# Kernel optimization log

Measured on AMD Instinct MI355X. Metric: run time of the kernel, lower is better.

Reference implementation:

```python
import jax, jax.numpy as jnp
import numpy as np

N = 128       # n_channels
B = 131072    # batch
C = np.float32(np.sqrt(0.5))  # 50/50 beamsplitter amplitude (c = s = sqrt(0.5))


def setup_inputs() -> dict:
    key = jax.random.key(0)
    k1, k2, k3, k4 = jax.random.split(key, 4)
    M = N * (N - 1) // 2
    return {
        "x_real": jax.random.normal(k1, (B, N), jnp.float32),
        "x_imag": jax.random.normal(k2, (B, N), jnp.float32),
        "mzi_phases": jax.random.normal(k3, (M * 2,), jnp.float32) * 0.1,
        "output_phases": jax.random.normal(k4, (N,), jnp.float32) * 0.1,
    }


def _construct_unitary(mzi_phases, output_phases):
    n = output_phases.shape[0]
    m = n * (n - 1) // 2
    # pair ordering matches the torch double loop: i ascending, then j > i (row-major triu)
    i_np, j_np = np.triu_indices(n, 1)
    i_idx = jnp.asarray(i_np, jnp.int32)
    j_idx = jnp.asarray(j_np, jnp.int32)
    ph = mzi_phases.reshape(m, 2)
    theta, phi = ph[:, 0], ph[:, 1]

    def step(U, xs):
        th, ph_, i, j = xs
        e_phi = jax.lax.complex(jnp.cos(ph_), jnp.sin(ph_))
        e_th = jax.lax.complex(jnp.cos(th), jnp.sin(th))
        ri = U[i]
        rj = U[j]
        # T_ij @ U touches only rows i and j (O(N) Givens row update)
        new_i = C * ri + (C * e_phi) * rj
        new_j = (C * e_th) * ri - (C * e_th * e_phi) * rj
        U = U.at[i].set(new_i).at[j].set(new_j)
        return U, None

    def chunk_body(U, xs_chunk):
        U, _ = jax.lax.scan(step, U, xs_chunk)
        return U, None

    # chunk the M sequential updates: M = (n-1) * (n//2) for even n;
    # checkpointing chunks keeps reverse-mode memory O(sqrt-ish) instead of O(M * N^2)
    n_chunks = n - 1
    cs = n // 2
    xs = (theta.reshape(n_chunks, cs), phi.reshape(n_chunks, cs),
          i_idx.reshape(n_chunks, cs), j_idx.reshape(n_chunks, cs))
    U0 = jnp.eye(n, dtype=jnp.complex64)
    U, _ = jax.lax.scan(jax.checkpoint(chunk_body), U0, xs)
    # output phase screen D @ U
    d = jax.lax.complex(jnp.cos(output_phases), jnp.sin(output_phases))
    return d[:, None] * U


def reference(x_real, x_imag, mzi_phases, output_phases):
    U = _construct_unitary(mzi_phases, output_phases)           # [N, N] complex64
    x = jax.lax.complex(x_real, x_imag)                          # [B, N] complex64
    # matmul(U, x.unsqueeze(-1)).squeeze(-1) == x @ U^T
    out = jnp.einsum('nm,bm->bn', U, x)                          # [B, N] complex64
    # ComplexDropout is identity in eval mode
    return out
```

## Files before the change

### kernel.cpp

```cpp
#include <hip/hip_runtime.h>
#include <hip/hip_bf16.h>

#define NDIM 128
#define BDIM 131072
#define NMZI 8128
#define NCHUNK 8
#define CSTEP (NMZI / NCHUNK)
#define NJG 8
#define NCOL 32
#define NLOC 16
static constexpr float CC = 0.70710678118654752440f;

typedef __attribute__((ext_vector_type(8))) short bf16x8;
typedef __attribute__((ext_vector_type(4))) float f32x4;

__device__ __align__(16) float2         g_V[NCHUNK * NDIM * NDIM];
__device__ __align__(16) float2         g_W[4 * NDIM * NDIM];
__device__ __align__(16) float2         g_Y[2 * NDIM * NDIM];
__device__ __align__(16) unsigned short g_TB[32 * NDIM * 8];
__device__ __align__(16) unsigned short g_Ur[16 * NDIM * 8];
__device__ __align__(16) unsigned short g_Ui[16 * NDIM * 8];

__device__ inline unsigned short f2bf(float f) {
    union { __hip_bfloat16 h; unsigned short u; } cv;
    cv.h = __float2bfloat16(f);
    return cv.u;
}

__global__ __launch_bounds__(256) void build_scan(const float* __restrict__ mzi) {
    __shared__ float2 Usm[NDIM][NCOL];
    __shared__ float4 phs[CSTEP];
    __shared__ float4 comp[NJG][NCOL];
    const int tid   = threadIdx.x;
    const int c     = tid & 31;
    const int g     = tid >> 5;
    const int col0  = blockIdx.x * NCOL;
    const int chunk = blockIdx.y;
    const int s0 = chunk * CSTEP, s1 = s0 + CSTEP;

    for (int k = g; k < NDIM; k += NJG)
        Usm[k][c] = make_float2((k == col0 + c) ? 1.f : 0.f, 0.f);
    const float2* mzp = (const float2*)mzi;
    for (int t = tid; t < CSTEP; t += 256) {
        const float2 mz = mzp[s0 + t];
        float sp, cp, st, ct;
        sincosf(mz.y, &sp, &cp);
        sincosf(mz.x, &st, &ct);
        phs[t] = make_float4(cp, sp, CC * ct, CC * st);
    }
    __syncthreads();

    int i = 0, base = 0;
    while (base + (NDIM - 1 - i) <= s0) { base += NDIM - 1 - i; ++i; }

    int s = s0;
    while (s < s1) {
        const int cnt  = NDIM - 1 - i;
        const int jA   = i + 1 + (s - base);
        const int L    = min(s1, base + cnt) - s;
        const int nloc = (L + NJG - 1) >> 3;
        const int myBeg = g * nloc;
        const int myN   = max(0, min(nloc, L - myBeg));
        const int pbase = s - s0;

        const float2 r0 = Usm[i][c];

        float2 treg[NLOC];
        float2 qth[NLOC];
        float  A = 1.f;
        float2 Bc = make_float2(0.f, 0.f);
        #pragma unroll
        for (int kk = 0; kk < NLOC; ++kk) {
            if (kk < myN) {
                const int off = myBeg + kk;
                const float4 q  = phs[pbase + off];
                const float2 rj = Usm[jA + off][c];
                const float tr = fmaf(q.x, rj.x, -q.y * rj.y);
                const float ti = fmaf(q.x, rj.y,  q.y * rj.x);
                treg[kk] = make_float2(tr, ti);
                qth[kk]  = make_float2(q.z, q.w);
                Bc.x = CC * (Bc.x + tr);
                Bc.y = CC * (Bc.y + ti);
                A *= CC;
            }
        }
        comp[g][c] = make_float4(A, Bc.x, Bc.y, 0.f);
        __syncthreads();

        float2 r = r0;
        for (int h = 0; h < g; ++h) {
            const float4 cm = comp[h][c];
            r.x = fmaf(cm.x, r.x, cm.y);
            r.y = fmaf(cm.x, r.y, cm.z);
        }

        #pragma unroll
        for (int kk = 0; kk < NLOC; ++kk) {
            if (kk < myN) {
                const float2 t = treg[kk];
                const float2 q = qth[kk];
                const float dr = r.x - t.x, di = r.y - t.y;
                const float njx = fmaf(q.x, dr, -q.y * di);
                const float njy = fmaf(q.x, di,  q.y * dr);
                Usm[jA + myBeg + kk][c] = make_float2(njx, njy);
                r.x = CC * (r.x + t.x);
                r.y = CC * (r.y + t.y);
            }
        }
        if (myN > 0 && (myBeg + myN == L))
            Usm[i][c] = r;
        __syncthreads();

        s += L;
        if (s == base + cnt) { base += cnt; ++i; }
    }

    float2* Vp = g_V + chunk * NDIM * NDIM;
    for (int k = g; k < NDIM; k += NJG)
        Vp[k * NDIM + col0 + c] = Usm[k][c];
}

__global__ __launch_bounds__(128) void compose(int level) {
    const int p = blockIdx.y, n = blockIdx.x, m = threadIdx.x;
    const float2* A; const float2* B; float2* Cout;
    if (level == 0) {
        A = g_V + (2 * p + 1) * NDIM * NDIM;
        B = g_V + (2 * p) * NDIM * NDIM;
        Cout = g_W + p * NDIM * NDIM;
    } else {
        A = g_W + (2 * p + 1) * NDIM * NDIM;
        B = g_W + (2 * p) * NDIM * NDIM;
        Cout = g_Y + p * NDIM * NDIM;
    }
    __shared__ float2 arow[NDIM];
    arow[m] = A[n * NDIM + m];
    __syncthreads();
    float cr = 0.f, ci = 0.f;
    #pragma unroll 8
    for (int k = 0; k < NDIM; ++k) {
        const float2 b = B[k * NDIM + m];
        const float2 a = arow[k];
        cr = fmaf(a.x, b.x, fmaf(-a.y, b.y, cr));
        ci = fmaf(a.x, b.y, fmaf( a.y, b.x, ci));
    }
    Cout[n * NDIM + m] = make_float2(cr, ci);
}

__global__ __launch_bounds__(128) void compose_final(const float* __restrict__ oph) {
    const int n = blockIdx.x, m = threadIdx.x;
    const float2* A = g_Y + NDIM * NDIM;
    const float2* B = g_Y;
    __shared__ float2 arow[NDIM];
    arow[m] = A[n * NDIM + m];
    __syncthreads();
    float cr = 0.f, ci = 0.f;
    #pragma unroll 8
    for (int k = 0; k < NDIM; ++k) {
        const float2 b = B[k * NDIM + m];
        const float2 a = arow[k];
        cr = fmaf(a.x, b.x, fmaf(-a.y, b.y, cr));
        ci = fmaf(a.x, b.y, fmaf( a.y, b.x, ci));
    }
    float ds, dc;
    sincosf(oph[n], &ds, &dc);
    const float vr = fmaf(cr, dc, -ci * ds);
    const float vi = fmaf(cr, ds,  ci * dc);
    const int kg = m >> 3, e = m & 7;
    g_TB[(kg * NDIM + n) * 8 + e]        = f2bf(vr);
    g_TB[((16 + kg) * NDIM + n) * 8 + e] = f2bf(-vi);
    g_Ur[(kg * NDIM + n) * 8 + e] = f2bf(vr);
    g_Ui[(kg * NDIM + n) * 8 + e] = f2bf(vi);
}

__global__ __launch_bounds__(256) void cmatmul0(const float* __restrict__ xr,
                                                const float* __restrict__ xi,
                                                float* __restrict__ out) {
    __shared__ __align__(16) char smX[4][8192];
    const int tid  = threadIdx.x;
    const int lane = tid & 63;
    const int w    = tid >> 6;
    const int r15  = lane & 15;
    const int kg4  = lane >> 4;
    const int l31  = lane & 31;
    const int lh   = lane >> 5;
    const int R    = blockIdx.x * 64 + w * 16;

    const float4* sre = (const float4*)(xr + (size_t)R * NDIM);
    const float4* sim = (const float4*)(xi + (size_t)R * NDIM);
    float4 G[16];
    #pragma unroll
    for (int p = 0; p < 8; ++p) G[p]     = sre[p * 64 + lane];
    #pragma unroll
    for (int p = 0; p < 8; ++p) G[8 + p] = sim[p * 64 + lane];

    char* buf = &smX[w][0];
    #pragma unroll
    for (int p = 0; p < 8; ++p) {
        const int row = 2 * p + lh;
        const int swz = (row & 7) << 4;
        uint2 v;
        v.x = ((unsigned)f2bf(G[p].y) << 16) | f2bf(G[p].x);
        v.y = ((unsigned)f2bf(G[p].w) << 16) | f2bf(G[p].z);
        *(uint2*)(buf + row * 512 + ((l31 * 8) ^ swz)) = v;
        v.x = ((unsigned)f2bf(G[8 + p].y) << 16) | f2bf(G[8 + p].x);
        v.y = ((unsigned)f2bf(G[8 + p].w) << 16) | f2bf(G[8 + p].z);
        *(uint2*)(buf + row * 512 + 256 + ((l31 * 8) ^ swz)) = v;
    }

    bf16x8 fx[8];
    const int rswz = (r15 & 7) << 4;
    #pragma unroll
    for (int kc = 0; kc < 8; ++kc) {
        const int off = (((kc & 3) * 64 + kg4 * 16) ^ rswz) + ((kc >= 4) ? 256 : 0);
        fx[kc] = *(const bf16x8*)(buf + r15 * 512 + off);
    }

    const bf16x8* gT = (const bf16x8*)g_TB;
    const size_t orow = (size_t)(R + r15) * NDIM;
    #pragma unroll
    for (int nt = 0; nt < 8; ++nt) {
        f32x4 a0 = {0.f, 0.f, 0.f, 0.f};
        f32x4 a1 = {0.f, 0.f, 0.f, 0.f};
        #pragma unroll
        for (int kc = 0; kc < 4; ++kc)
            a0 = __builtin_amdgcn_mfma_f32_16x16x32_bf16(
                gT[(kc * 4 + kg4) * NDIM + nt * 16 + r15], fx[kc], a0, 0, 0, 0);
        #pragma unroll
        for (int kc = 4; kc < 8; ++kc)
            a1 = __builtin_amdgcn_mfma_f32_16x16x32_bf16(
                gT[(kc * 4 + kg4) * NDIM + nt * 16 + r15], fx[kc], a1, 0, 0, 0);
        const f32x4 s = a0 + a1;
        *(float4*)(out + orow + nt * 16 + kg4 * 4) =
            make_float4(s[0], s[1], s[2], s[3]);
    }
}

__global__ __launch_bounds__(256) void cmatmul1(const float* __restrict__ xr,
                                                const float* __restrict__ xi,
                                                ushort2* __restrict__ outp) {
    const int lane  = threadIdx.x & 63;
    const int w     = threadIdx.x >> 6;
    const int btile = blockIdx.x * 64 + w * 16;
    const int r15   = lane & 15;
    const int kg4   = lane >> 4;
    const int bload = btile + r15;

    const bf16x8* Ur = (const bf16x8*)g_Ur;
    const bf16x8* Ui = (const bf16x8*)g_Ui;
    const float* xrp = xr + (size_t)bload * NDIM;
    const float* xip = xi + (size_t)bload * NDIM;

    bf16x8 ar[4], ai[4], ain[4];
    #pragma unroll
    for (int kc = 0; kc < 4; ++kc) {
        const int k0 = kc * 32 + kg4 * 8;
        float4 rlo = *(const float4*)(xrp + k0);
        float4 rhi = *(const float4*)(xrp + k0 + 4);
        float4 ilo = *(const float4*)(xip + k0);
        float4 ihi = *(const float4*)(xip + k0 + 4);
        bf16x8 vr, vi, vn;
        vr[0] = (short)f2bf(rlo.x); vr[1] = (short)f2bf(rlo.y);
        vr[2] = (short)f2bf(rlo.z); vr[3] = (short)f2bf(rlo.w);
        vr[4] = (short)f2bf(rhi.x); vr[5] = (short)f2bf(rhi.y);
        vr[6] = (short)f2bf(rhi.z); vr[7] = (short)f2bf(rhi.w);
        vi[0] = (short)f2bf(ilo.x); vi[1] = (short)f2bf(ilo.y);
        vi[2] = (short)f2bf(ilo.z); vi[3] = (short)f2bf(ilo.w);
        vi[4] = (short)f2bf(ihi.x); vi[5] = (short)f2bf(ihi.y);
        vi[6] = (short)f2bf(ihi.z); vi[7] = (short)f2bf(ihi.w);
        #pragma unroll
        for (int e = 0; e < 8; ++e) vn[e] = (short)(vi[e] ^ 0x8000);
        ar[kc] = vr; ai[kc] = vi; ain[kc] = vn;
    }

    #pragma unroll
    for (int nt = 0; nt < 8; ++nt) {
        f32x4 accR = {0.f, 0.f, 0.f, 0.f};
        f32x4 accI = {0.f, 0.f, 0.f, 0.f};
        #pragma unroll
        for (int kc = 0; kc < 4; ++kc) {
            const int kg = kc * 4 + kg4;
            bf16x8 br = Ur[kg * NDIM + nt * 16 + r15];
            bf16x8 bi = Ui[kg * NDIM + nt * 16 + r15];
            accR = __builtin_amdgcn_mfma_f32_16x16x32_bf16(ar[kc],  br, accR, 0, 0, 0);
            accR = __builtin_amdgcn_mfma_f32_16x16x32_bf16(ain[kc], bi, accR, 0, 0, 0);
            accI = __builtin_amdgcn_mfma_f32_16x16x32_bf16(ar[kc],  bi, accI, 0, 0, 0);
            accI = __builtin_amdgcn_mfma_f32_16x16x32_bf16(ai[kc],  br, accI, 0, 0, 0);
        }
        const int n    = nt * 16 + r15;
        const int brow = btile + kg4 * 4;
        #pragma unroll
        for (int r = 0; r < 4; ++r)
            outp[(size_t)(brow + r) * NDIM + n] = make_ushort2(f2bf(accR[r]), f2bf(accI[r]));
    }
}

extern "C" void kernel_launch(void* const* d_in, const int* in_sizes, int n_in,
                              void* d_out, int out_size, void* d_ws, size_t ws_size,
                              hipStream_t stream) {
    const float* xr  = (const float*)d_in[0];
    const float* xi  = (const float*)d_in[1];
    const float* mzi = (const float*)d_in[2];
    const float* oph = (const float*)d_in[3];

    build_scan<<<dim3(4, NCHUNK), dim3(256), 0, stream>>>(mzi);
    compose<<<dim3(NDIM, 4), dim3(128), 0, stream>>>(0);
    compose<<<dim3(NDIM, 2), dim3(128), 0, stream>>>(1);
    compose_final<<<dim3(NDIM), dim3(128), 0, stream>>>(oph);
    if (out_size == BDIM * NDIM) {
        cmatmul0<<<dim3(BDIM / 64), dim3(256), 0, stream>>>(xr, xi, (float*)d_out);
    } else {
        cmatmul1<<<dim3(BDIM / 64), dim3(256), 0, stream>>>(xr, xi, (ushort2*)d_out);
    }
}
```

Baseline: 122.7 us.

## Split MZI scan into more chunks and use nontemporal loads/stores in matmul

Doubles the number of parallel scan chunks in the unitary build from 8 to 16, adding one more level to the pairwise compose tree, so the serial Givens-rotation chain per block is half as long. The complex matmul kernel also switches its input loads and output stores to nontemporal builtins to reduce cache pollution on the streamed data. The cost is an extra compose launch and a larger intermediate buffer.

After: 128.5 us. +4.7%, slower.

```diff
diff --git a/kernel.cpp b/kernel.cpp
--- a/kernel.cpp
+++ b/kernel.cpp
@@ -4,7 +4,7 @@
 #define NDIM 128
 #define BDIM 131072
 #define NMZI 8128
-#define NCHUNK 8
+#define NCHUNK 16
 #define CSTEP (NMZI / NCHUNK)
 #define NJG 8
 #define NCOL 32
@@ -15,7 +15,8 @@
 typedef __attribute__((ext_vector_type(4))) float f32x4;
 
 __device__ __align__(16) float2         g_V[NCHUNK * NDIM * NDIM];
-__device__ __align__(16) float2         g_W[4 * NDIM * NDIM];
+__device__ __align__(16) float2         g_W8[8 * NDIM * NDIM];
+__device__ __align__(16) float2         g_W4[4 * NDIM * NDIM];
 __device__ __align__(16) float2         g_Y[2 * NDIM * NDIM];
 __device__ __align__(16) unsigned short g_TB[32 * NDIM * 8];
 __device__ __align__(16) unsigned short g_Ur[16 * NDIM * 8];
@@ -126,10 +127,14 @@
     if (level == 0) {
         A = g_V + (2 * p + 1) * NDIM * NDIM;
         B = g_V + (2 * p) * NDIM * NDIM;
-        Cout = g_W + p * NDIM * NDIM;
+        Cout = g_W8 + p * NDIM * NDIM;
+    } else if (level == 1) {
+        A = g_W8 + (2 * p + 1) * NDIM * NDIM;
+        B = g_W8 + (2 * p) * NDIM * NDIM;
+        Cout = g_W4 + p * NDIM * NDIM;
     } else {
-        A = g_W + (2 * p + 1) * NDIM * NDIM;
-        B = g_W + (2 * p) * NDIM * NDIM;
+        A = g_W4 + (2 * p + 1) * NDIM * NDIM;
+        B = g_W4 + (2 * p) * NDIM * NDIM;
         Cout = g_Y + p * NDIM * NDIM;
     }
     __shared__ float2 arow[NDIM];
@@ -185,13 +190,13 @@
     const int lh   = lane >> 5;
     const int R    = blockIdx.x * 64 + w * 16;
 
-    const float4* sre = (const float4*)(xr + (size_t)R * NDIM);
-    const float4* sim = (const float4*)(xi + (size_t)R * NDIM);
-    float4 G[16];
-    #pragma unroll
-    for (int p = 0; p < 8; ++p) G[p]     = sre[p * 64 + lane];
-    #pragma unroll
-    for (int p = 0; p < 8; ++p) G[8 + p] = sim[p * 64 + lane];
+    const f32x4* sre = (const f32x4*)(xr + (size_t)R * NDIM);
+    const f32x4* sim = (const f32x4*)(xi + (size_t)R * NDIM);
+    f32x4 G[16];
+    #pragma unroll
+    for (int p = 0; p < 8; ++p) G[p]     = __builtin_nontemporal_load(sre + p * 64 + lane);
+    #pragma unroll
+    for (int p = 0; p < 8; ++p) G[8 + p] = __builtin_nontemporal_load(sim + p * 64 + lane);
 
     char* buf = &smX[w][0];
     #pragma unroll
@@ -199,11 +204,11 @@
         const int row = 2 * p + lh;
         const int swz = (row & 7) << 4;
         uint2 v;
-        v.x = ((unsigned)f2bf(G[p].y) << 16) | f2bf(G[p].x);
-        v.y = ((unsigned)f2bf(G[p].w) << 16) | f2bf(G[p].z);
+        v.x = ((unsigned)f2bf(G[p][1]) << 16) | f2bf(G[p][0]);
+        v.y = ((unsigned)f2bf(G[p][3]) << 16) | f2bf(G[p][2]);
         *(uint2*)(buf + row * 512 + ((l31 * 8) ^ swz)) = v;
-        v.x = ((unsigned)f2bf(G[8 + p].y) << 16) | f2bf(G[8 + p].x);
-        v.y = ((unsigned)f2bf(G[8 + p].w) << 16) | f2bf(G[8 + p].z);
+        v.x = ((unsigned)f2bf(G[8 + p][1]) << 16) | f2bf(G[8 + p][0]);
+        v.y = ((unsigned)f2bf(G[8 + p][3]) << 16) | f2bf(G[8 + p][2]);
         *(uint2*)(buf + row * 512 + 256 + ((l31 * 8) ^ swz)) = v;
     }
 
@@ -230,8 +235,7 @@
             a1 = __builtin_amdgcn_mfma_f32_16x16x32_bf16(
                 gT[(kc * 4 + kg4) * NDIM + nt * 16 + r15], fx[kc], a1, 0, 0, 0);
         const f32x4 s = a0 + a1;
-        *(float4*)(out + orow + nt * 16 + kg4 * 4) =
-            make_float4(s[0], s[1], s[2], s[3]);
+        __builtin_nontemporal_store(s, (f32x4*)(out + orow + nt * 16 + kg4 * 4));
     }
 }
 
@@ -303,8 +307,9 @@
     const float* oph = (const float*)d_in[3];
 
     build_scan<<<dim3(4, NCHUNK), dim3(256), 0, stream>>>(mzi);
-    compose<<<dim3(NDIM, 4), dim3(128), 0, stream>>>(0);
-    compose<<<dim3(NDIM, 2), dim3(128), 0, stream>>>(1);
+    compose<<<dim3(NDIM, 8), dim3(128), 0, stream>>>(0);
+    compose<<<dim3(NDIM, 4), dim3(128), 0, stream>>>(1);
+    compose<<<dim3(NDIM, 2), dim3(128), 0, stream>>>(2);
     compose_final<<<dim3(NDIM), dim3(128), 0, stream>>>(oph);
     if (out_size == BDIM * NDIM) {
         cmatmul0<<<dim3(BDIM / 64), dim3(256), 0, stream>>>(xr, xi, (float*)d_out);
```
